# Kernel optimization log

Hardware: AMD Instinct MI355X
Metric: run time of the kernel (lower is better)

## Reference

```python
import jax, jax.numpy as jnp
import numpy as np

T, B, C = 2048, 8, 512
OUT = 512
NE = 16
TOPK = 2
LOSS_SCALE = 0.01
NEG_INF = 1.0e6  # module uses -1000000.0 for masked logits


def setup_inputs() -> dict:
    key = jax.random.key(0)
    k = jax.random.split(key, 4)
    a_assign = np.sqrt(6.0 / (C + NE)).astype(np.float32)  # xavier_uniform for Linear(C, NE)
    a_w1 = np.float32(np.sqrt(6.0) / (C + OUT))            # dynamic_init_method == 1
    return {
        "x": jax.random.normal(k[0], (T, B, C), dtype=jnp.float32),
        "assign_w": jax.random.uniform(k[1], (NE, C), minval=-a_assign, maxval=a_assign, dtype=jnp.float32),
        "assign_b": jnp.zeros((NE,), dtype=jnp.float32),
        "pw_w1": jax.random.uniform(k[2], (NE, OUT * C), minval=-a_w1, maxval=a_w1, dtype=jnp.float32),
        "bias_w": jnp.zeros((OUT, C), dtype=jnp.float32),  # pw_bias weight initialized to 0
        "bias_b": jnp.zeros((OUT,), dtype=jnp.float32),
    }


def reference(x, assign_w, assign_b, pw_w1, bias_w, bias_b):
    # key=None path of ConditionalDLFactorized18.forward, eval mode, tau=0 -> softmax gating.
    tokens = x.reshape(T * B, C)
    # Gating energies: Linear(key_dim, ne)
    energies = tokens @ assign_w.T + assign_b  # [TB, ne]
    # keeptopk_masked: set entries below k-th largest to -1e6
    topv, _ = jax.lax.top_k(energies, TOPK)
    energies = jnp.where(energies < topv[..., TOPK - 1:TOPK], -NEG_INF, energies)
    resp = jax.nn.softmax(energies, axis=-1)  # [TB, ne]
    # Importance/commitment loss (torch.std is unbiased -> ddof=1)
    importance = resp.sum(axis=0)  # [ne]
    loss = (LOSS_SCALE * jnp.std(importance, ddof=1) / jnp.mean(importance)).reshape(1)
    # Algebraically-equivalent reorder of (resp @ pw_w1).view(T,B,out,in) @ x:
    # apply each expert's matrix to the token first, then mix with resp.
    W = pw_w1.reshape(NE, OUT, C)
    expert_out = jnp.einsum("nc,eoc->neo", tokens, W)      # [TB, ne, out]
    y = jnp.einsum("ne,neo->no", resp, expert_out)          # [TB, out]
    y = y.reshape(T, B, OUT)
    # dynamic bias: pw_bias(x0) = x0 @ bias_w.T + bias_b
    y = y + x @ bias_w.T + bias_b
    return y, loss
```

## Files before the change

kernel.cpp:

```cpp
#include <hip/hip_runtime.h>
#include <hip/hip_bf16.h>

#define TB 16384
#define CDIM 512
#define OUTD 512
#define NE 16
#define NE_TOT 17
#define LOSS_SCALE 0.01f
#define BM 128
#define BN 128
#define BK 64
#define MAX_SCHED 144
#define MAXFLAG 8192
#define MARGIN 1e-3f

typedef __bf16 bf16_t;
typedef bf16_t bf16x8 __attribute__((ext_vector_type(8)));
typedef float f32x4 __attribute__((ext_vector_type(4)));
typedef unsigned short ushort4_t __attribute__((ext_vector_type(4)));
typedef unsigned short ushort8_t __attribute__((ext_vector_type(8)));

__device__ __forceinline__ unsigned short f2bf(float f) {
    unsigned int u = __float_as_uint(f);
    u += 0x7fffu + ((u >> 16) & 1u);
    return (unsigned short)(u >> 16);
}
__device__ __forceinline__ float bf2f(unsigned short h) {
    return __uint_as_float((unsigned int)h << 16);
}

__device__ __forceinline__ void async_copy16(void* lds, const void* g) {
    __builtin_amdgcn_global_load_lds(
        (const __attribute__((address_space(1))) unsigned int*)g,
        (__attribute__((address_space(3))) unsigned int*)lds, 16, 0, 0);
}

__global__ __launch_bounds__(256) void k_prep(
    const float* __restrict__ aw, unsigned short* __restrict__ awhl,
    int* cnt0, int* cnt1, float* importance, int* nflag, int* wflag)
{
    int t = threadIdx.x;
    if (t < NE) { cnt0[t] = 0; cnt1[t] = 0; importance[t] = 0.f; }
    if (t == 0) { *nflag = 0; *wflag = 0; }
    for (int i = t; i < NE * CDIM; i += 256) {
        float f = aw[i];
        unsigned short h = f2bf(f);
        float r = f - bf2f(h);
        awhl[i] = h;
        awhl[NE * CDIM + i] = f2bf(r);
    }
}

__global__ void k_wconv(const float* __restrict__ pw, const float* __restrict__ bw,
                        unsigned short* __restrict__ wbf, int* __restrict__ wflag) {
    long i = (long)blockIdx.x * 256 + threadIdx.x;
    const long NPW = (long)NE * OUTD * CDIM / 4;
    const long NTOT = (long)NE_TOT * OUTD * CDIM / 4;
    if (i >= NTOT) return;
    const float* src = (i < NPW) ? (pw + i * 4) : (bw + (i - NPW) * 4);
    float4 v = *(const float4*)src;
    ushort4_t o;
    o[0] = f2bf(v.x); o[1] = f2bf(v.y); o[2] = f2bf(v.z); o[3] = f2bf(v.w);
    *(ushort4_t*)(wbf + i * 4) = o;
    if (i >= NPW && (v.x != 0.f || v.y != 0.f || v.z != 0.f || v.w != 0.f))
        atomicOr(wflag, 1);
}

__global__ __launch_bounds__(256) void k_gate(
    const float* __restrict__ x, const unsigned short* __restrict__ awhl,
    const float* __restrict__ ab, unsigned short* __restrict__ xbf,
    int* __restrict__ dec, float2* __restrict__ respd,
    int* __restrict__ flaglist, int* __restrict__ nflag, float* __restrict__ importance)
{
    __shared__ float imp_s[NE];
    int tid = threadIdx.x;
    if (tid < NE) imp_s[tid] = 0.f;
    __syncthreads();

    int wv = tid >> 6, l = tid & 63;
    int n0 = blockIdx.x * 64 + wv * 16;
    int e = l & 15;
    int kg = l >> 4;

    const float* xrow = x + (size_t)(n0 + e) * CDIM + kg * 8;
    unsigned short* xbrow = xbf + (size_t)(n0 + e) * CDIM + kg * 8;
    const unsigned short* whiP = awhl + e * CDIM + kg * 8;
    const unsigned short* wloP = whiP + NE * CDIM;

    f32x4 acc = (f32x4){0.f, 0.f, 0.f, 0.f};
    #pragma unroll 4
    for (int ks = 0; ks < 16; ++ks) {
        float4 v0 = *(const float4*)(xrow + ks * 32);
        float4 v1 = *(const float4*)(xrow + ks * 32 + 4);
        ushort8_t hx, lx;
        #define CVT(idx, f) { unsigned short h_ = f2bf(f); hx[idx] = h_; \
                              float r_ = (f) - bf2f(h_); lx[idx] = f2bf(r_); }
        CVT(0, v0.x) CVT(1, v0.y) CVT(2, v0.z) CVT(3, v0.w)
        CVT(4, v1.x) CVT(5, v1.y) CVT(6, v1.z) CVT(7, v1.w)
        #undef CVT
        *(ushort8_t*)(xbrow + ks * 32) = hx;
        ushort8_t wh8 = *(const ushort8_t*)(whiP + ks * 32);
        ushort8_t wl8 = *(const ushort8_t*)(wloP + ks * 32);
        bf16x8 ah = *(bf16x8*)&hx, al = *(bf16x8*)&lx;
        bf16x8 bh = *(bf16x8*)&wh8, bl = *(bf16x8*)&wl8;
        acc = __builtin_amdgcn_mfma_f32_16x16x32_bf16(al, bh, acc, 0, 0, 0);
        acc = __builtin_amdgcn_mfma_f32_16x16x32_bf16(ah, bl, acc, 0, 0, 0);
        acc = __builtin_amdgcn_mfma_f32_16x16x32_bf16(ah, bh, acc, 0, 0, 0);
    }
    float bias = ab[e];
    f32x4 E;
    #pragma unroll
    for (int q = 0; q < 4; ++q) E[q] = acc[q] + bias;

    f32x4 m1 = E, m2, m3;
    #pragma unroll
    for (int q = 0; q < 4; ++q) { m2[q] = -3.4e38f; m3[q] = -3.4e38f; }
    #pragma unroll
    for (int off = 1; off <= 8; off <<= 1) {
        #pragma unroll
        for (int q = 0; q < 4; ++q) {
            float o1 = __shfl_xor(m1[q], off, 64);
            float o2 = __shfl_xor(m2[q], off, 64);
            float o3 = __shfl_xor(m3[q], off, 64);
            float M1 = fmaxf(m1[q], o1), x1 = fminf(m1[q], o1);
            float h2 = fmaxf(m2[q], o2), l2 = fminf(m2[q], o2);
            float M2 = fmaxf(x1, h2), x2 = fminf(x1, h2);
            float M3 = fmaxf(fmaxf(x2, l2), fmaxf(m3[q], o3));
            m1[q] = M1; m2[q] = M2; m3[q] = M3;
        }
    }
    f32x4 p, z;
    #pragma unroll
    for (int q = 0; q < 4; ++q) p[q] = (E[q] >= m2[q]) ? expf(E[q] - m1[q]) : 0.f;
    z = p;
    #pragma unroll
    for (int off = 1; off <= 8; off <<= 1)
        #pragma unroll
        for (int q = 0; q < 4; ++q) z[q] += __shfl_xor(z[q], off, 64);
    f32x4 resp;
    #pragma unroll
    for (int q = 0; q < 4; ++q) resp[q] = p[q] / z[q];

    int grp = l >> 4;
    int elo_q[4], ehi_q[4];
    float rlo_q[4], rhi_q[4];
    #pragma unroll
    for (int q = 0; q < 4; ++q) {
        unsigned long long mq = __ballot(p[q] > 0.f);
        unsigned int sub = (unsigned int)((mq >> (grp * 16)) & 0xffffULL);
        elo_q[q] = __builtin_ctz(sub);
        ehi_q[q] = 31 - __builtin_clz(sub);
        rlo_q[q] = __shfl(resp[q], grp * 16 + elo_q[q], 64);
        rhi_q[q] = __shfl(resp[q], grp * 16 + ehi_q[q], 64);
    }
    if ((l & 15) == 0) {
        #pragma unroll
        for (int q = 0; q < 4; ++q) {
            int n = n0 + grp * 4 + q;
            dec[n] = elo_q[q] | (ehi_q[q] << 8);
            respd[n] = make_float2(rlo_q[q], rhi_q[q]);
            if (m2[q] - m3[q] < MARGIN) {
                int ix = atomicAdd(nflag, 1);
                if (ix < MAXFLAG) flaglist[ix] = n;
            }
        }
    }
    float s = resp[0] + resp[1] + resp[2] + resp[3];
    s += __shfl_xor(s, 16, 64);
    s += __shfl_xor(s, 32, 64);
    if (l < 16) atomicAdd(&imp_s[e], s);
    __syncthreads();
    if (tid < NE) unsafeAtomicAdd(&importance[tid], imp_s[tid]);
}

__global__ __launch_bounds__(256) void k_repair(
    const float* __restrict__ x, const float* __restrict__ aw, const float* __restrict__ ab,
    const int* __restrict__ flaglist, const int* __restrict__ nflag,
    int* __restrict__ dec, float2* __restrict__ respd, float* __restrict__ importance)
{
    __shared__ double part[16][17];
    __shared__ double Ed[16];
    int tid = threadIdx.x;
    int e = tid >> 4, p = tid & 15;
    int nf = *nflag; if (nf > MAXFLAG) nf = MAXFLAG;
    for (int fi = blockIdx.x; fi < nf; fi += gridDim.x) {
        int n = flaglist[fi];
        const float* xp = x + (size_t)n * CDIM + p * 32;
        const float* wp = aw + e * CDIM + p * 32;
        double acc = 0.0;
        for (int j = 0; j < 32; ++j) acc = fma((double)xp[j], (double)wp[j], acc);
        part[e][p] = acc;
        __syncthreads();
        if (tid < 16) {
            double s = (double)ab[tid];
            for (int q = 0; q < 16; ++q) s += part[tid][q];
            Ed[tid] = s;
        }
        __syncthreads();
        if (tid == 0) {
            double m1 = -1e300, m2 = -1e300, m3 = -1e300;
            for (int q = 0; q < 16; ++q) {
                double v = Ed[q];
                if (v > m1) { m3 = m2; m2 = m1; m1 = v; }
                else if (v > m2) { m3 = m2; m2 = v; }
                else if (v > m3) { m3 = v; }
            }
            int elo = -1, ehi = -1;
            for (int q = 0; q < 16; ++q)
                if (Ed[q] >= m2) { if (elo < 0) elo = q; else ehi = q; }
            double plo = exp(Ed[elo] - m1), phi = exp(Ed[ehi] - m1);
            double zz = plo + phi;
            float rlo = (float)(plo / zz), rhi = (float)(phi / zz);
            int od = dec[n]; float2 orr = respd[n];
            unsafeAtomicAdd(&importance[od & 0xff], -orr.x);
            unsafeAtomicAdd(&importance[(od >> 8) & 0xff], -orr.y);
            unsafeAtomicAdd(&importance[elo], rlo);
            unsafeAtomicAdd(&importance[ehi], rhi);
            dec[n] = elo | (ehi << 8);
            respd[n] = make_float2(rlo, rhi);
        }
        __syncthreads();
    }
}

__global__ __launch_bounds__(256) void k_build(
    const int* __restrict__ dec, int* __restrict__ cnt0, int* __restrict__ cnt1,
    int* __restrict__ idx0, int* __restrict__ idx1)
{
    __shared__ int l0[NE], l1[NE], b0[NE], b1[NE];
    int tid = threadIdx.x;
    if (tid < NE) { l0[tid] = 0; l1[tid] = 0; }
    __syncthreads();
    int n = blockIdx.x * 256 + tid;
    int d = dec[n];
    int elo = d & 0xff, ehi = (d >> 8) & 0xff;
    int p0 = atomicAdd(&l0[elo], 1);
    int p1 = atomicAdd(&l1[ehi], 1);
    __syncthreads();
    if (tid < NE) {
        b0[tid] = atomicAdd(&cnt0[tid], l0[tid]);
        b1[tid] = atomicAdd(&cnt1[tid], l1[tid]);
    }
    __syncthreads();
    idx0[elo * TB + b0[elo] + p0] = n;
    idx1[ehi * TB + b1[ehi] + p1] = n;
}

__global__ void k_finish(const float* __restrict__ importance, float* __restrict__ out_loss,
                         const int* __restrict__ cnt0, const int* __restrict__ cnt1,
                         int* __restrict__ sched0, int* __restrict__ sched1,
                         int* __restrict__ sn0, int* __restrict__ sn1) {
    int l = threadIdx.x;
    if (l < 64) {
        float v = (l < NE) ? importance[l] : 0.f;
        float s = v;
        #pragma unroll
        for (int off = 8; off >= 1; off >>= 1) s += __shfl_xor(s, off, 64);
        float mean = s / 16.f;
        float d = (l < NE) ? (v - mean) : 0.f;
        float ss = d * d;
        #pragma unroll
        for (int off = 8; off >= 1; off >>= 1) ss += __shfl_xor(ss, off, 64);
        if (l == 0) {
            float stdv = sqrtf(ss / 15.f);
            out_loss[0] = LOSS_SCALE * stdv / mean;
        }
    } else if (l == 64) {
        int p = 0;
        for (int e = 0; e < NE; ++e) {
            int nb = (cnt0[e] + BM - 1) / BM;
            for (int i = 0; i < nb; ++i) sched0[p++] = (e << 16) | i;
        }
        *sn0 = p;
    } else if (l == 65) {
        int p = 0;
        for (int e = 0; e < NE; ++e) {
            int nb = (cnt1[e] + BM - 1) / BM;
            for (int i = 0; i < nb; ++i) sched1[p++] = (e << 16) | i;
        }
        *sn1 = p;
    }
}

template<int RANK>
__global__ __launch_bounds__(256) void k_gemm(
    const unsigned short* __restrict__ xbf, const unsigned short* __restrict__ wbf,
    const int* __restrict__ cnts, const int* __restrict__ idx,
    const float2* __restrict__ respd, const int* __restrict__ sched,
    const int* __restrict__ sn, const float* __restrict__ bias_b, float* __restrict__ y)
{
    if ((int)blockIdx.y >= *sn) return;
    int s = sched[blockIdx.y];
    int e = s >> 16, m0 = (s & 0xffff) * BM, cnt = cnts[e];
    int n0 = blockIdx.x * BN;
    int tid = threadIdx.x;
    int wave = tid >> 6, lane = tid & 63;
    int wm = wave >> 1, wn = wave & 1;
    int fr = lane & 15, fq = lane >> 4;

    __shared__ unsigned short As[BM * BK];
    __shared__ unsigned short Bs[BN * BK];

    const int* my_idx = idx + e * TB;

    f32x4 acc[4][4];
    #pragma unroll
    for (int m = 0; m < 4; ++m)
        #pragma unroll
        for (int nn = 0; nn < 4; ++nn) acc[m][nn] = (f32x4){0.f, 0.f, 0.f, 0.f};

    int srow = wave * 8 + (lane >> 3);
    int cg = lane & 7;
    const unsigned short* aSrc[4];
    const unsigned short* bSrc[4];
    #pragma unroll
    for (int c = 0; c < 4; ++c) {
        int row = c * 32 + srow;
        int sc = (cg ^ (row & 7)) * 8;
        int rr = m0 + row; if (rr >= cnt) rr = cnt - 1;
        int tok = my_idx[rr];
        aSrc[c] = xbf + (size_t)tok * CDIM + sc;
        bSrc[c] = wbf + ((size_t)e * OUTD + n0 + row) * CDIM + sc;
    }
    for (int k0 = 0; k0 < CDIM; k0 += BK) {
        __syncthreads();
        #pragma unroll
        for (int c = 0; c < 4; ++c) {
            async_copy16(&As[(c * 32 + wave * 8) * BK], aSrc[c] + k0);
            async_copy16(&Bs[(c * 32 + wave * 8) * BK], bSrc[c] + k0);
        }
        __syncthreads();
        #pragma unroll
        for (int ss = 0; ss < 2; ++ss) {
            bf16x8 af[4], bv[4];
            #pragma unroll
            for (int m = 0; m < 4; ++m) {
                int row = wm * 64 + m * 16 + fr;
                int ch = ((ss * 4 + fq) ^ (row & 7)) * 8;
                af[m] = *(const bf16x8*)(&As[row * BK + ch]);
            }
            #pragma unroll
            for (int nn = 0; nn < 4; ++nn) {
                int row = wn * 64 + nn * 16 + fr;
                int ch = ((ss * 4 + fq) ^ (row & 7)) * 8;
                bv[nn] = *(const bf16x8*)(&Bs[row * BK + ch]);
            }
            #pragma unroll
            for (int m = 0; m < 4; ++m)
                #pragma unroll
                for (int nn = 0; nn < 4; ++nn)
                    acc[m][nn] = __builtin_amdgcn_mfma_f32_16x16x32_bf16(af[m], bv[nn], acc[m][nn], 0, 0, 0);
        }
    }

    float bb[4];
    if (RANK == 0) {
        #pragma unroll
        for (int nn = 0; nn < 4; ++nn) bb[nn] = bias_b[n0 + wn * 64 + nn * 16 + fr];
    }
    #pragma unroll
    for (int m = 0; m < 4; ++m)
        #pragma unroll
        for (int q = 0; q < 4; ++q) {
            int r = m0 + wm * 64 + m * 16 + fq * 4 + q;
            if (r < cnt) {
                int tok = my_idx[r];
                float2 rp = respd[tok];
                float w = (RANK == 0) ? rp.x : rp.y;
                float* yrow = y + (size_t)tok * OUTD + n0 + wn * 64 + fr;
                #pragma unroll
                for (int nn = 0; nn < 4; ++nn) {
                    if (RANK == 0) yrow[nn * 16] = fmaf(w, acc[m][nn][q], bb[nn]);
                    else           yrow[nn * 16] += w * acc[m][nn][q];
                }
            }
        }
}

__global__ __launch_bounds__(256) void k_dense(
    const unsigned short* __restrict__ xbf, const unsigned short* __restrict__ wbf,
    const int* __restrict__ wflag, float* __restrict__ y)
{
    if (*wflag == 0) return;
    int e = NE;
    int m0 = blockIdx.y * BM;
    int n0 = blockIdx.x * BN;
    int tid = threadIdx.x;
    int wave = tid >> 6, lane = tid & 63;
    int wm = wave >> 1, wn = wave & 1;
    int fr = lane & 15, fq = lane >> 4;

    __shared__ unsigned short As[BM * BK];
    __shared__ unsigned short Bs[BN * BK];

    f32x4 acc[4][4];
    #pragma unroll
    for (int m = 0; m < 4; ++m)
        #pragma unroll
        for (int nn = 0; nn < 4; ++nn) acc[m][nn] = (f32x4){0.f, 0.f, 0.f, 0.f};

    int srow = wave * 8 + (lane >> 3);
    int cg = lane & 7;
    const unsigned short* aSrc[4];
    const unsigned short* bSrc[4];
    #pragma unroll
    for (int c = 0; c < 4; ++c) {
        int row = c * 32 + srow;
        int sc = (cg ^ (row & 7)) * 8;
        aSrc[c] = xbf + (size_t)(m0 + row) * CDIM + sc;
        bSrc[c] = wbf + ((size_t)e * OUTD + n0 + row) * CDIM + sc;
    }
    for (int k0 = 0; k0 < CDIM; k0 += BK) {
        __syncthreads();
        #pragma unroll
        for (int c = 0; c < 4; ++c) {
            async_copy16(&As[(c * 32 + wave * 8) * BK], aSrc[c] + k0);
            async_copy16(&Bs[(c * 32 + wave * 8) * BK], bSrc[c] + k0);
        }
        __syncthreads();
        #pragma unroll
        for (int ss = 0; ss < 2; ++ss) {
            bf16x8 af[4], bv[4];
            #pragma unroll
            for (int m = 0; m < 4; ++m) {
                int row = wm * 64 + m * 16 + fr;
                int ch = ((ss * 4 + fq) ^ (row & 7)) * 8;
                af[m] = *(const bf16x8*)(&As[row * BK + ch]);
            }
            #pragma unroll
            for (int nn = 0; nn < 4; ++nn) {
                int row = wn * 64 + nn * 16 + fr;
                int ch = ((ss * 4 + fq) ^ (row & 7)) * 8;
                bv[nn] = *(const bf16x8*)(&Bs[row * BK + ch]);
            }
            #pragma unroll
            for (int m = 0; m < 4; ++m)
                #pragma unroll
                for (int nn = 0; nn < 4; ++nn)
                    acc[m][nn] = __builtin_amdgcn_mfma_f32_16x16x32_bf16(af[m], bv[nn], acc[m][nn], 0, 0, 0);
        }
    }
    #pragma unroll
    for (int m = 0; m < 4; ++m)
        #pragma unroll
        for (int q = 0; q < 4; ++q) {
            int r = m0 + wm * 64 + m * 16 + fq * 4 + q;
            float* yrow = y + (size_t)r * OUTD + n0 + wn * 64 + fr;
            #pragma unroll
            for (int nn = 0; nn < 4; ++nn) yrow[nn * 16] += acc[m][nn][q];
        }
}

extern "C" void kernel_launch(void* const* d_in, const int* in_sizes, int n_in,
                              void* d_out, int out_size, void* d_ws, size_t ws_size,
                              hipStream_t stream) {
    const float* x        = (const float*)d_in[0];
    const float* assign_w = (const float*)d_in[1];
    const float* assign_b = (const float*)d_in[2];
    const float* pw_w1    = (const float*)d_in[3];
    const float* bias_w   = (const float*)d_in[4];
    const float* bias_b   = (const float*)d_in[5];
    float* y    = (float*)d_out;
    float* loss = y + (size_t)TB * OUTD;

    char* ws = (char*)d_ws;
    unsigned short* xbf  = (unsigned short*)(ws);
    unsigned short* wbf  = (unsigned short*)(ws + 16777216);
    int*    idx0      = (int*)   (ws + 25690112);
    int*    idx1      = (int*)   (ws + 26738688);
    int*    dec       = (int*)   (ws + 27787264);
    float2* respd     = (float2*)(ws + 27852800);
    int*    flaglist  = (int*)   (ws + 27983872);
    unsigned short* awhl = (unsigned short*)(ws + 28016640);
    char*   misc      = ws + 28049408;
    int*    cnt0      = (int*)   (misc + 0);
    int*    cnt1      = (int*)   (misc + 64);
    float*  importance= (float*) (misc + 128);
    int*    nflag     = (int*)   (misc + 192);
    int*    wflag     = (int*)   (misc + 196);
    int*    sn0       = (int*)   (misc + 200);
    int*    sn1       = (int*)   (misc + 204);
    int*    sched0    = (int*)   (misc + 256);
    int*    sched1    = (int*)   (misc + 896);

    k_prep<<<1, 256, 0, stream>>>(assign_w, awhl, cnt0, cnt1, importance, nflag, wflag);
    k_wconv<<<(NE_TOT * OUTD * CDIM / 4 + 255) / 256, 256, 0, stream>>>(pw_w1, bias_w, wbf, wflag);
    k_gate<<<TB / 64, 256, 0, stream>>>(x, awhl, assign_b, xbf, dec, respd,
                                        flaglist, nflag, importance);
    k_repair<<<32, 256, 0, stream>>>(x, assign_w, assign_b, flaglist, nflag,
                                     dec, respd, importance);
    k_build<<<TB / 256, 256, 0, stream>>>(dec, cnt0, cnt1, idx0, idx1);
    k_finish<<<1, 128, 0, stream>>>(importance, loss, cnt0, cnt1, sched0, sched1, sn0, sn1);
    k_gemm<0><<<dim3(OUTD / BN, MAX_SCHED), 256, 0, stream>>>(
        xbf, wbf, cnt0, idx0, respd, sched0, sn0, bias_b, y);
    k_gemm<1><<<dim3(OUTD / BN, MAX_SCHED), 256, 0, stream>>>(
        xbf, wbf, cnt1, idx1, respd, sched1, sn1, bias_b, y);
    k_dense<<<dim3(OUTD / BN, TB / BM), 256, 0, stream>>>(xbf, wbf, wflag, y);
}
```

Before: 130.6 us.

## Group tokens by expert pair and fuse both expert GEMMs into one kernel

Tokens are bucketed by their (top1, top2) expert pair using count, scan and scatter kernels instead of per-rank expert lists. A single GEMM kernel then computes both experts' outputs for each tile, reusing the gathered activation rows, and writes y once. This removes the second GEMM launch and its read-modify-write pass over y. It also adds double-buffered LDS staging to overlap loads with MFMA work. With up to 240 possible pairs the tiles are less full, so more padded rows are wasted, and the kernel holds two accumulator sets, which raises register pressure.

New measurement: 172.2 us. 1.32x slower.

```diff
diff --git a/kernel.cpp b/kernel.cpp
--- a/kernel.cpp
+++ b/kernel.cpp
@@ -10,7 +10,7 @@
 #define BM 128
 #define BN 128
 #define BK 64
-#define MAX_SCHED 144
+#define MAX_SCHED_P 320
 #define MAXFLAG 8192
 #define MARGIN 1e-3f
 
@@ -37,10 +37,11 @@
 
 __global__ __launch_bounds__(256) void k_prep(
     const float* __restrict__ aw, unsigned short* __restrict__ awhl,
-    int* cnt0, int* cnt1, float* importance, int* nflag, int* wflag)
+    int* pair_cnt, float* importance, int* nflag, int* wflag)
 {
     int t = threadIdx.x;
-    if (t < NE) { cnt0[t] = 0; cnt1[t] = 0; importance[t] = 0.f; }
+    pair_cnt[t] = 0;
+    if (t < NE) importance[t] = 0.f;
     if (t == 0) { *nflag = 0; *wflag = 0; }
     for (int i = t; i < NE * CDIM; i += 256) {
         float f = aw[i];
@@ -223,35 +224,42 @@
     }
 }
 
-__global__ __launch_bounds__(256) void k_build(
-    const int* __restrict__ dec, int* __restrict__ cnt0, int* __restrict__ cnt1,
-    int* __restrict__ idx0, int* __restrict__ idx1)
-{
-    __shared__ int l0[NE], l1[NE], b0[NE], b1[NE];
+__global__ __launch_bounds__(256) void k_count(
+    const int* __restrict__ dec, int* __restrict__ pair_cnt)
+{
+    __shared__ int c_s[256];
     int tid = threadIdx.x;
-    if (tid < NE) { l0[tid] = 0; l1[tid] = 0; }
+    c_s[tid] = 0;
     __syncthreads();
     int n = blockIdx.x * 256 + tid;
     int d = dec[n];
-    int elo = d & 0xff, ehi = (d >> 8) & 0xff;
-    int p0 = atomicAdd(&l0[elo], 1);
-    int p1 = atomicAdd(&l1[ehi], 1);
+    int pid = ((d & 0xff) << 4) | ((d >> 8) & 0xff);
+    atomicAdd(&c_s[pid], 1);
     __syncthreads();
-    if (tid < NE) {
-        b0[tid] = atomicAdd(&cnt0[tid], l0[tid]);
-        b1[tid] = atomicAdd(&cnt1[tid], l1[tid]);
-    }
-    __syncthreads();
-    idx0[elo * TB + b0[elo] + p0] = n;
-    idx1[ehi * TB + b1[ehi] + p1] = n;
-}
-
-__global__ void k_finish(const float* __restrict__ importance, float* __restrict__ out_loss,
-                         const int* __restrict__ cnt0, const int* __restrict__ cnt1,
-                         int* __restrict__ sched0, int* __restrict__ sched1,
-                         int* __restrict__ sn0, int* __restrict__ sn1) {
-    int l = threadIdx.x;
-    if (l < 64) {
+    if (c_s[tid] > 0) atomicAdd(&pair_cnt[tid], c_s[tid]);
+}
+
+__global__ void k_scan(const int* __restrict__ pair_cnt, int* __restrict__ pair_base,
+                       int* __restrict__ pair_fill, int* __restrict__ sched,
+                       int* __restrict__ sn,
+                       const float* __restrict__ importance, float* __restrict__ out_loss)
+{
+    __shared__ int base_s[256];
+    int t = threadIdx.x;
+    if (t == 0) {
+        int p = 0;
+        for (int i = 0; i < 256; ++i) { base_s[i] = p; p += pair_cnt[i]; }
+    }
+    if (t == 1) {
+        int ns = 0;
+        for (int i = 0; i < 256; ++i) {
+            int nb = (pair_cnt[i] + BM - 1) / BM;
+            for (int b = 0; b < nb; ++b) sched[ns++] = (i << 8) | b;
+        }
+        *sn = ns;
+    }
+    if (t >= 64 && t < 128) {
+        int l = t - 64;
         float v = (l < NE) ? importance[l] : 0.f;
         float s = v;
         #pragma unroll
@@ -265,54 +273,58 @@
             float stdv = sqrtf(ss / 15.f);
             out_loss[0] = LOSS_SCALE * stdv / mean;
         }
-    } else if (l == 64) {
-        int p = 0;
-        for (int e = 0; e < NE; ++e) {
-            int nb = (cnt0[e] + BM - 1) / BM;
-            for (int i = 0; i < nb; ++i) sched0[p++] = (e << 16) | i;
-        }
-        *sn0 = p;
-    } else if (l == 65) {
-        int p = 0;
-        for (int e = 0; e < NE; ++e) {
-            int nb = (cnt1[e] + BM - 1) / BM;
-            for (int i = 0; i < nb; ++i) sched1[p++] = (e << 16) | i;
-        }
-        *sn1 = p;
-    }
-}
-
-template<int RANK>
-__global__ __launch_bounds__(256) void k_gemm(
+    }
+    __syncthreads();
+    pair_base[t] = base_s[t];
+    pair_fill[t] = base_s[t];
+}
+
+__global__ __launch_bounds__(256) void k_scatter(
+    const int* __restrict__ dec, int* __restrict__ pair_fill, int* __restrict__ pidx)
+{
+    int n = blockIdx.x * 256 + threadIdx.x;
+    int d = dec[n];
+    int pid = ((d & 0xff) << 4) | ((d >> 8) & 0xff);
+    int slot = atomicAdd(&pair_fill[pid], 1);
+    pidx[slot] = n;
+}
+
+__global__ __launch_bounds__(256) void k_gemm_pair(
     const unsigned short* __restrict__ xbf, const unsigned short* __restrict__ wbf,
-    const int* __restrict__ cnts, const int* __restrict__ idx,
-    const float2* __restrict__ respd, const int* __restrict__ sched,
-    const int* __restrict__ sn, const float* __restrict__ bias_b, float* __restrict__ y)
+    const int* __restrict__ pair_cnt, const int* __restrict__ pair_base,
+    const int* __restrict__ pidx, const float2* __restrict__ respd,
+    const int* __restrict__ sched, const int* __restrict__ sn,
+    const float* __restrict__ bias_b, float* __restrict__ y)
 {
     if ((int)blockIdx.y >= *sn) return;
     int s = sched[blockIdx.y];
-    int e = s >> 16, m0 = (s & 0xffff) * BM, cnt = cnts[e];
+    int pid = s >> 8, mb = s & 0xff;
+    int e0 = pid >> 4, e1 = pid & 15;
+    int cnt = pair_cnt[pid];
+    int m0 = mb * BM;
+    const int* my_idx = pidx + pair_base[pid];
     int n0 = blockIdx.x * BN;
     int tid = threadIdx.x;
     int wave = tid >> 6, lane = tid & 63;
     int wm = wave >> 1, wn = wave & 1;
     int fr = lane & 15, fq = lane >> 4;
 
-    __shared__ unsigned short As[BM * BK];
-    __shared__ unsigned short Bs[BN * BK];
-
-    const int* my_idx = idx + e * TB;
-
-    f32x4 acc[4][4];
+    __shared__ unsigned short As[2][BM * BK];
+    __shared__ unsigned short Bs[2][BM * BK];
+
+    f32x4 acc0[4][4], acc1[4][4];
     #pragma unroll
     for (int m = 0; m < 4; ++m)
         #pragma unroll
-        for (int nn = 0; nn < 4; ++nn) acc[m][nn] = (f32x4){0.f, 0.f, 0.f, 0.f};
+        for (int nn = 0; nn < 4; ++nn) {
+            acc0[m][nn] = (f32x4){0.f, 0.f, 0.f, 0.f};
+            acc1[m][nn] = (f32x4){0.f, 0.f, 0.f, 0.f};
+        }
 
     int srow = wave * 8 + (lane >> 3);
     int cg = lane & 7;
     const unsigned short* aSrc[4];
-    const unsigned short* bSrc[4];
+    size_t bOff[4];
     #pragma unroll
     for (int c = 0; c < 4; ++c) {
         int row = c * 32 + srow;
@@ -320,16 +332,19 @@
         int rr = m0 + row; if (rr >= cnt) rr = cnt - 1;
         int tok = my_idx[rr];
         aSrc[c] = xbf + (size_t)tok * CDIM + sc;
-        bSrc[c] = wbf + ((size_t)e * OUTD + n0 + row) * CDIM + sc;
-    }
-    for (int k0 = 0; k0 < CDIM; k0 += BK) {
-        __syncthreads();
+        bOff[c] = (size_t)(n0 + row) * CDIM + sc;
+    }
+    const unsigned short* wb0 = wbf + (size_t)e0 * OUTD * CDIM;
+    const unsigned short* wb1 = wbf + (size_t)e1 * OUTD * CDIM;
+
+    auto stagef = [&](int buf, const unsigned short* wb, int k0) {
         #pragma unroll
         for (int c = 0; c < 4; ++c) {
-            async_copy16(&As[(c * 32 + wave * 8) * BK], aSrc[c] + k0);
-            async_copy16(&Bs[(c * 32 + wave * 8) * BK], bSrc[c] + k0);
-        }
-        __syncthreads();
+            async_copy16(&As[buf][(c * 32 + wave * 8) * BK], aSrc[c] + k0);
+            async_copy16(&Bs[buf][(c * 32 + wave * 8) * BK], wb + bOff[c] + k0);
+        }
+    };
+    auto compute = [&](int cb, f32x4 (&acc)[4][4]) {
         #pragma unroll
         for (int ss = 0; ss < 2; ++ss) {
             bf16x8 af[4], bv[4];
@@ -337,13 +352,13 @@
             for (int m = 0; m < 4; ++m) {
                 int row = wm * 64 + m * 16 + fr;
                 int ch = ((ss * 4 + fq) ^ (row & 7)) * 8;
-                af[m] = *(const bf16x8*)(&As[row * BK + ch]);
+                af[m] = *(const bf16x8*)(&As[cb][row * BK + ch]);
             }
             #pragma unroll
             for (int nn = 0; nn < 4; ++nn) {
                 int row = wn * 64 + nn * 16 + fr;
                 int ch = ((ss * 4 + fq) ^ (row & 7)) * 8;
-                bv[nn] = *(const bf16x8*)(&Bs[row * BK + ch]);
+                bv[nn] = *(const bf16x8*)(&Bs[cb][row * BK + ch]);
             }
             #pragma unroll
             for (int m = 0; m < 4; ++m)
@@ -351,13 +366,28 @@
                 for (int nn = 0; nn < 4; ++nn)
                     acc[m][nn] = __builtin_amdgcn_mfma_f32_16x16x32_bf16(af[m], bv[nn], acc[m][nn], 0, 0, 0);
         }
+    };
+
+    stagef(0, wb0, 0);
+    __syncthreads();
+    int cur = 0;
+    for (int t = 0; t < 8; ++t) {
+        if (t < 7) stagef(cur ^ 1, wb0, (t + 1) * BK);
+        else       stagef(cur ^ 1, wb1, 0);
+        compute(cur, acc0);
+        __syncthreads();
+        cur ^= 1;
+    }
+    for (int t = 0; t < 8; ++t) {
+        if (t < 7) stagef(cur ^ 1, wb1, (t + 1) * BK);
+        compute(cur, acc1);
+        __syncthreads();
+        cur ^= 1;
     }
 
     float bb[4];
-    if (RANK == 0) {
-        #pragma unroll
-        for (int nn = 0; nn < 4; ++nn) bb[nn] = bias_b[n0 + wn * 64 + nn * 16 + fr];
-    }
+    #pragma unroll
+    for (int nn = 0; nn < 4; ++nn) bb[nn] = bias_b[n0 + wn * 64 + nn * 16 + fr];
     #pragma unroll
     for (int m = 0; m < 4; ++m)
         #pragma unroll
@@ -366,13 +396,11 @@
             if (r < cnt) {
                 int tok = my_idx[r];
                 float2 rp = respd[tok];
-                float w = (RANK == 0) ? rp.x : rp.y;
                 float* yrow = y + (size_t)tok * OUTD + n0 + wn * 64 + fr;
                 #pragma unroll
-                for (int nn = 0; nn < 4; ++nn) {
-                    if (RANK == 0) yrow[nn * 16] = fmaf(w, acc[m][nn][q], bb[nn]);
-                    else           yrow[nn * 16] += w * acc[m][nn][q];
-                }
+                for (int nn = 0; nn < 4; ++nn)
+                    yrow[nn * 16] = fmaf(rp.x, acc0[m][nn][q],
+                                    fmaf(rp.y, acc1[m][nn][q], bb[nn]));
             }
         }
 }
@@ -391,7 +419,7 @@
     int fr = lane & 15, fq = lane >> 4;
 
     __shared__ unsigned short As[BM * BK];
-    __shared__ unsigned short Bs[BN * BK];
+    __shared__ unsigned short Bs[BM * BK];
 
     f32x4 acc[4][4];
     #pragma unroll
@@ -466,34 +494,32 @@
     char* ws = (char*)d_ws;
     unsigned short* xbf  = (unsigned short*)(ws);
     unsigned short* wbf  = (unsigned short*)(ws + 16777216);
-    int*    idx0      = (int*)   (ws + 25690112);
-    int*    idx1      = (int*)   (ws + 26738688);
+    int*    pidx      = (int*)   (ws + 25690112);
     int*    dec       = (int*)   (ws + 27787264);
     float2* respd     = (float2*)(ws + 27852800);
     int*    flaglist  = (int*)   (ws + 27983872);
     unsigned short* awhl = (unsigned short*)(ws + 28016640);
     char*   misc      = ws + 28049408;
-    int*    cnt0      = (int*)   (misc + 0);
-    int*    cnt1      = (int*)   (misc + 64);
-    float*  importance= (float*) (misc + 128);
-    int*    nflag     = (int*)   (misc + 192);
-    int*    wflag     = (int*)   (misc + 196);
-    int*    sn0       = (int*)   (misc + 200);
-    int*    sn1       = (int*)   (misc + 204);
-    int*    sched0    = (int*)   (misc + 256);
-    int*    sched1    = (int*)   (misc + 896);
-
-    k_prep<<<1, 256, 0, stream>>>(assign_w, awhl, cnt0, cnt1, importance, nflag, wflag);
+    int*    pair_cnt  = (int*)   (misc + 0);
+    int*    pair_base = (int*)   (misc + 1024);
+    int*    pair_fill = (int*)   (misc + 2048);
+    float*  importance= (float*) (misc + 3072);
+    int*    nflag     = (int*)   (misc + 3136);
+    int*    wflag     = (int*)   (misc + 3140);
+    int*    sn        = (int*)   (misc + 3144);
+    int*    sched     = (int*)   (misc + 3200);
+
+    k_prep<<<1, 256, 0, stream>>>(assign_w, awhl, pair_cnt, importance, nflag, wflag);
     k_wconv<<<(NE_TOT * OUTD * CDIM / 4 + 255) / 256, 256, 0, stream>>>(pw_w1, bias_w, wbf, wflag);
     k_gate<<<TB / 64, 256, 0, stream>>>(x, awhl, assign_b, xbf, dec, respd,
                                         flaglist, nflag, importance);
     k_repair<<<32, 256, 0, stream>>>(x, assign_w, assign_b, flaglist, nflag,
                                      dec, respd, importance);
-    k_build<<<TB / 256, 256, 0, stream>>>(dec, cnt0, cnt1, idx0, idx1);
-    k_finish<<<1, 128, 0, stream>>>(importance, loss, cnt0, cnt1, sched0, sched1, sn0, sn1);
-    k_gemm<0><<<dim3(OUTD / BN, MAX_SCHED), 256, 0, stream>>>(
-        xbf, wbf, cnt0, idx0, respd, sched0, sn0, bias_b, y);
-    k_gemm<1><<<dim3(OUTD / BN, MAX_SCHED), 256, 0, stream>>>(
-        xbf, wbf, cnt1, idx1, respd, sched1, sn1, bias_b, y);
+    k_count<<<TB / 256, 256, 0, stream>>>(dec, pair_cnt);
+    k_scan<<<1, 256, 0, stream>>>(pair_cnt, pair_base, pair_fill, sched, sn,
+                                  importance, loss);
+    k_scatter<<<TB / 256, 256, 0, stream>>>(dec, pair_fill, pidx);
+    k_gemm_pair<<<dim3(OUTD / BN, MAX_SCHED_P), 256, 0, stream>>>(
+        xbf, wbf, pair_cnt, pair_base, pidx, respd, sched, sn, bias_b, y);
     k_dense<<<dim3(OUTD / BN, TB / BM), 256, 0, stream>>>(xbf, wbf, wflag, y);
 }
```

## Double-buffer LDS tiles and halve N tile in expert GEMM kernels

Applied to the files above, without the earlier changes.

Both the routed expert GEMM and the dense GEMM now use two LDS buffers, so the async copy of the next K slice is issued before the current slice is computed. This removes one barrier per iteration and overlaps global loads with MFMA work. BN is cut from 128 to 64, which doubles the block count and halves the accumulator registers per wave. The cost is that each block reads the gathered A rows twice as often relative to its output, and per-block arithmetic intensity drops.

Result: slower. 142.4 us (+9.0%).

```diff
diff --git a/kernel.cpp b/kernel.cpp
--- a/kernel.cpp
+++ b/kernel.cpp
@@ -8,7 +8,7 @@
 #define NE_TOT 17
 #define LOSS_SCALE 0.01f
 #define BM 128
-#define BN 128
+#define BN 64
 #define BK 64
 #define MAX_SCHED 144
 #define MAXFLAG 8192
@@ -298,21 +298,21 @@
     int wm = wave >> 1, wn = wave & 1;
     int fr = lane & 15, fq = lane >> 4;
 
-    __shared__ unsigned short As[BM * BK];
-    __shared__ unsigned short Bs[BN * BK];
+    __shared__ unsigned short As[2][BM * BK];
+    __shared__ unsigned short Bs[2][BN * BK];
 
     const int* my_idx = idx + e * TB;
 
-    f32x4 acc[4][4];
+    f32x4 acc[4][2];
     #pragma unroll
     for (int m = 0; m < 4; ++m)
         #pragma unroll
-        for (int nn = 0; nn < 4; ++nn) acc[m][nn] = (f32x4){0.f, 0.f, 0.f, 0.f};
+        for (int nn = 0; nn < 2; ++nn) acc[m][nn] = (f32x4){0.f, 0.f, 0.f, 0.f};
 
     int srow = wave * 8 + (lane >> 3);
     int cg = lane & 7;
     const unsigned short* aSrc[4];
-    const unsigned short* bSrc[4];
+    const unsigned short* bSrc[2];
     #pragma unroll
     for (int c = 0; c < 4; ++c) {
         int row = c * 32 + srow;
@@ -320,43 +320,61 @@
         int rr = m0 + row; if (rr >= cnt) rr = cnt - 1;
         int tok = my_idx[rr];
         aSrc[c] = xbf + (size_t)tok * CDIM + sc;
+    }
+    #pragma unroll
+    for (int c = 0; c < 2; ++c) {
+        int row = c * 32 + srow;
+        int sc = (cg ^ (row & 7)) * 8;
         bSrc[c] = wbf + ((size_t)e * OUTD + n0 + row) * CDIM + sc;
     }
-    for (int k0 = 0; k0 < CDIM; k0 += BK) {
-        __syncthreads();
-        #pragma unroll
-        for (int c = 0; c < 4; ++c) {
-            async_copy16(&As[(c * 32 + wave * 8) * BK], aSrc[c] + k0);
-            async_copy16(&Bs[(c * 32 + wave * 8) * BK], bSrc[c] + k0);
-        }
-        __syncthreads();
+
+    auto stagef = [&](int buf, int k0) {
+        #pragma unroll
+        for (int c = 0; c < 4; ++c)
+            async_copy16(&As[buf][(c * 32 + wave * 8) * BK], aSrc[c] + k0);
+        #pragma unroll
+        for (int c = 0; c < 2; ++c)
+            async_copy16(&Bs[buf][(c * 32 + wave * 8) * BK], bSrc[c] + k0);
+    };
+    auto compute = [&](int cb) {
         #pragma unroll
         for (int ss = 0; ss < 2; ++ss) {
-            bf16x8 af[4], bv[4];
+            bf16x8 af[4], bv[2];
             #pragma unroll
             for (int m = 0; m < 4; ++m) {
                 int row = wm * 64 + m * 16 + fr;
                 int ch = ((ss * 4 + fq) ^ (row & 7)) * 8;
-                af[m] = *(const bf16x8*)(&As[row * BK + ch]);
-            }
-            #pragma unroll
-            for (int nn = 0; nn < 4; ++nn) {
-                int row = wn * 64 + nn * 16 + fr;
+                af[m] = *(const bf16x8*)(&As[cb][row * BK + ch]);
+            }
+            #pragma unroll
+            for (int nn = 0; nn < 2; ++nn) {
+                int row = wn * 32 + nn * 16 + fr;
                 int ch = ((ss * 4 + fq) ^ (row & 7)) * 8;
-                bv[nn] = *(const bf16x8*)(&Bs[row * BK + ch]);
+                bv[nn] = *(const bf16x8*)(&Bs[cb][row * BK + ch]);
             }
             #pragma unroll
             for (int m = 0; m < 4; ++m)
                 #pragma unroll
-                for (int nn = 0; nn < 4; ++nn)
+                for (int nn = 0; nn < 2; ++nn)
                     acc[m][nn] = __builtin_amdgcn_mfma_f32_16x16x32_bf16(af[m], bv[nn], acc[m][nn], 0, 0, 0);
         }
-    }
-
-    float bb[4];
+    };
+
+    stagef(0, 0);
+    __syncthreads();
+    int cur = 0;
+    #pragma unroll
+    for (int t = 0; t < 8; ++t) {
+        if (t < 7) stagef(cur ^ 1, (t + 1) * BK);
+        compute(cur);
+        __syncthreads();
+        cur ^= 1;
+    }
+
+    float bb[2];
     if (RANK == 0) {
         #pragma unroll
-        for (int nn = 0; nn < 4; ++nn) bb[nn] = bias_b[n0 + wn * 64 + nn * 16 + fr];
+        for (int nn = 0; nn < 2; ++nn) bb[nn] = bias_b[n0 + wn * 32 + nn * 16 + fr];
     }
     #pragma unroll
     for (int m = 0; m < 4; ++m)
@@ -367,9 +385,9 @@
                 int tok = my_idx[r];
                 float2 rp = respd[tok];
                 float w = (RANK == 0) ? rp.x : rp.y;
-                float* yrow = y + (size_t)tok * OUTD + n0 + wn * 64 + fr;
+                float* yrow = y + (size_t)tok * OUTD + n0 + wn * 32 + fr;
                 #pragma unroll
-                for (int nn = 0; nn < 4; ++nn) {
+                for (int nn = 0; nn < 2; ++nn) {
                     if (RANK == 0) yrow[nn * 16] = fmaf(w, acc[m][nn][q], bb[nn]);
                     else           yrow[nn * 16] += w * acc[m][nn][q];
                 }
@@ -390,64 +408,80 @@
     int wm = wave >> 1, wn = wave & 1;
     int fr = lane & 15, fq = lane >> 4;
 
-    __shared__ unsigned short As[BM * BK];
-    __shared__ unsigned short Bs[BN * BK];
-
-    f32x4 acc[4][4];
+    __shared__ unsigned short As[2][BM * BK];
+    __shared__ unsigned short Bs[2][BN * BK];
+
+    f32x4 acc[4][2];
     #pragma unroll
     for (int m = 0; m < 4; ++m)
         #pragma unroll
-        for (int nn = 0; nn < 4; ++nn) acc[m][nn] = (f32x4){0.f, 0.f, 0.f, 0.f};
+        for (int nn = 0; nn < 2; ++nn) acc[m][nn] = (f32x4){0.f, 0.f, 0.f, 0.f};
 
     int srow = wave * 8 + (lane >> 3);
     int cg = lane & 7;
     const unsigned short* aSrc[4];
-    const unsigned short* bSrc[4];
+    const unsigned short* bSrc[2];
     #pragma unroll
     for (int c = 0; c < 4; ++c) {
         int row = c * 32 + srow;
         int sc = (cg ^ (row & 7)) * 8;
         aSrc[c] = xbf + (size_t)(m0 + row) * CDIM + sc;
+    }
+    #pragma unroll
+    for (int c = 0; c < 2; ++c) {
+        int row = c * 32 + srow;
+        int sc = (cg ^ (row & 7)) * 8;
         bSrc[c] = wbf + ((size_t)e * OUTD + n0 + row) * CDIM + sc;
     }
-    for (int k0 = 0; k0 < CDIM; k0 += BK) {
-        __syncthreads();
-        #pragma unroll
-        for (int c = 0; c < 4; ++c) {
-            async_copy16(&As[(c * 32 + wave * 8) * BK], aSrc[c] + k0);
-            async_copy16(&Bs[(c * 32 + wave * 8) * BK], bSrc[c] + k0);
-        }
-        __syncthreads();
+    auto stagef = [&](int buf, int k0) {
+        #pragma unroll
+        for (int c = 0; c < 4; ++c)
+            async_copy16(&As[buf][(c * 32 + wave * 8) * BK], aSrc[c] + k0);
+        #pragma unroll
+        for (int c = 0; c < 2; ++c)
+            async_copy16(&Bs[buf][(c * 32 + wave * 8) * BK], bSrc[c] + k0);
+    };
+    auto compute = [&](int cb) {
         #pragma unroll
         for (int ss = 0; ss < 2; ++ss) {
-            bf16x8 af[4], bv[4];
+            bf16x8 af[4], bv[2];
             #pragma unroll
             for (int m = 0; m < 4; ++m) {
                 int row = wm * 64 + m * 16 + fr;
                 int ch = ((ss * 4 + fq) ^ (row & 7)) * 8;
-                af[m] = *(const bf16x8*)(&As[row * BK + ch]);
-            }
-            #pragma unroll
-            for (int nn = 0; nn < 4; ++nn) {
-                int row = wn * 64 + nn * 16 + fr;
+                af[m] = *(const bf16x8*)(&As[cb][row * BK + ch]);
+            }
+            #pragma unroll
+            for (int nn = 0; nn < 2; ++nn) {
+                int row = wn * 32 + nn * 16 + fr;
                 int ch = ((ss * 4 + fq) ^ (row & 7)) * 8;
-                bv[nn] = *(const bf16x8*)(&Bs[row * BK + ch]);
+                bv[nn] = *(const bf16x8*)(&Bs[cb][row * BK + ch]);
             }
             #pragma unroll
             for (int m = 0; m < 4; ++m)
                 #pragma unroll
-                for (int nn = 0; nn < 4; ++nn)
+                for (int nn = 0; nn < 2; ++nn)
                     acc[m][nn] = __builtin_amdgcn_mfma_f32_16x16x32_bf16(af[m], bv[nn], acc[m][nn], 0, 0, 0);
         }
+    };
+    stagef(0, 0);
+    __syncthreads();
+    int cur = 0;
+    #pragma unroll
+    for (int t = 0; t < 8; ++t) {
+        if (t < 7) stagef(cur ^ 1, (t + 1) * BK);
+        compute(cur);
+        __syncthreads();
+        cur ^= 1;
     }
     #pragma unroll
     for (int m = 0; m < 4; ++m)
         #pragma unroll
         for (int q = 0; q < 4; ++q) {
             int r = m0 + wm * 64 + m * 16 + fq * 4 + q;
-            float* yrow = y + (size_t)r * OUTD + n0 + wn * 64 + fr;
-            #pragma unroll
-            for (int nn = 0; nn < 4; ++nn) yrow[nn * 16] += acc[m][nn][q];
+            float* yrow = y + (size_t)r * OUTD + n0 + wn * 32 + fr;
+            #pragma unroll
+            for (int nn = 0; nn < 2; ++nn) yrow[nn * 16] += acc[m][nn][q];
         }
 }
 
```

## Pipeline expert GEMM with 4-stage async LDS buffers and smaller tiles

Applied to the files above, without the earlier changes.

Rewrites the grouped expert GEMM to use a 4-buffer async-copy pipeline with explicit vmcnt waits and a single barrier per K step, in place of the load-sync-compute loop. The tile shrinks from 128x128x64 to 128x64x32, which doubles the block count along N. The grid is transposed so that schedule entries sharing a weight tile run adjacently. The dense bias-path kernel becomes a mode of the same template. The aim is to overlap global loads with MFMA work and raise occupancy, at the cost of more loads of the gathered A rows per output and smaller per-block reuse.

New measurement: 135.8 us. +4.0%, slower.

```diff
diff --git a/kernel.cpp b/kernel.cpp
--- a/kernel.cpp
+++ b/kernel.cpp
@@ -8,8 +8,9 @@
 #define NE_TOT 17
 #define LOSS_SCALE 0.01f
 #define BM 128
-#define BN 128
-#define BK 64
+#define BN 64
+#define BK 32
+#define NSTEP 16
 #define MAX_SCHED 144
 #define MAXFLAG 8192
 #define MARGIN 1e-3f
@@ -282,81 +283,100 @@
     }
 }
 
-template<int RANK>
+template<int MODE>
 __global__ __launch_bounds__(256) void k_gemm(
     const unsigned short* __restrict__ xbf, const unsigned short* __restrict__ wbf,
     const int* __restrict__ cnts, const int* __restrict__ idx,
     const float2* __restrict__ respd, const int* __restrict__ sched,
-    const int* __restrict__ sn, const float* __restrict__ bias_b, float* __restrict__ y)
+    const int* __restrict__ sn, const int* __restrict__ wflag,
+    const float* __restrict__ bias_b, float* __restrict__ y)
 {
-    if ((int)blockIdx.y >= *sn) return;
-    int s = sched[blockIdx.y];
-    int e = s >> 16, m0 = (s & 0xffff) * BM, cnt = cnts[e];
-    int n0 = blockIdx.x * BN;
+    int e, m0, cnt;
+    const int* my_idx = nullptr;
+    if (MODE == 2) {
+        if (*wflag == 0) return;
+        e = NE; m0 = blockIdx.x * BM; cnt = TB;
+    } else {
+        if ((int)blockIdx.x >= *sn) return;
+        int s = sched[blockIdx.x];
+        e = s >> 16; m0 = (s & 0xffff) * BM; cnt = cnts[e];
+        my_idx = idx + e * TB;
+    }
+    int n0 = blockIdx.y * BN;
     int tid = threadIdx.x;
     int wave = tid >> 6, lane = tid & 63;
     int wm = wave >> 1, wn = wave & 1;
     int fr = lane & 15, fq = lane >> 4;
 
-    __shared__ unsigned short As[BM * BK];
-    __shared__ unsigned short Bs[BN * BK];
-
-    const int* my_idx = idx + e * TB;
-
-    f32x4 acc[4][4];
+    __shared__ unsigned short As[4][BM * BK];
+    __shared__ unsigned short Bs[4][BN * BK];
+
+    f32x4 acc[4][2];
     #pragma unroll
     for (int m = 0; m < 4; ++m)
         #pragma unroll
-        for (int nn = 0; nn < 4; ++nn) acc[m][nn] = (f32x4){0.f, 0.f, 0.f, 0.f};
-
-    int srow = wave * 8 + (lane >> 3);
-    int cg = lane & 7;
-    const unsigned short* aSrc[4];
-    const unsigned short* bSrc[4];
-    #pragma unroll
-    for (int c = 0; c < 4; ++c) {
-        int row = c * 32 + srow;
-        int sc = (cg ^ (row & 7)) * 8;
-        int rr = m0 + row; if (rr >= cnt) rr = cnt - 1;
-        int tok = my_idx[rr];
-        aSrc[c] = xbf + (size_t)tok * CDIM + sc;
-        bSrc[c] = wbf + ((size_t)e * OUTD + n0 + row) * CDIM + sc;
-    }
-    for (int k0 = 0; k0 < CDIM; k0 += BK) {
-        __syncthreads();
-        #pragma unroll
-        for (int c = 0; c < 4; ++c) {
-            async_copy16(&As[(c * 32 + wave * 8) * BK], aSrc[c] + k0);
-            async_copy16(&Bs[(c * 32 + wave * 8) * BK], bSrc[c] + k0);
-        }
-        __syncthreads();
-        #pragma unroll
-        for (int ss = 0; ss < 2; ++ss) {
-            bf16x8 af[4], bv[4];
+        for (int nn = 0; nn < 2; ++nn) acc[m][nn] = (f32x4){0.f, 0.f, 0.f, 0.f};
+
+    int rl = lane >> 2, cc = lane & 3;
+    int swz = (cc ^ (rl & 3)) * 8;
+    int rowA0 = wave * 32 + rl;
+    int rowA1 = rowA0 + 16;
+    int tok0, tok1;
+    if (MODE == 2) { tok0 = m0 + rowA0; tok1 = m0 + rowA1; }
+    else {
+        int rr0 = m0 + rowA0; if (rr0 >= cnt) rr0 = cnt - 1;
+        int rr1 = m0 + rowA1; if (rr1 >= cnt) rr1 = cnt - 1;
+        tok0 = my_idx[rr0]; tok1 = my_idx[rr1];
+    }
+    const unsigned short* aS0 = xbf + (size_t)tok0 * CDIM + swz;
+    const unsigned short* aS1 = xbf + (size_t)tok1 * CDIM + swz;
+    const unsigned short* bS0 = wbf + ((size_t)e * OUTD + n0 + wave * 16 + rl) * CDIM + swz;
+
+    unsigned short* dA0 = &As[0][(wave * 32) * BK];
+    unsigned short* dA1 = &As[0][(wave * 32 + 16) * BK];
+    unsigned short* dB0 = &Bs[0][(wave * 16) * BK];
+    const int ASTRIDE = BM * BK, BSTRIDE = BN * BK;
+
+    auto stage = [&](int buf, int t) {
+        async_copy16(dA0 + buf * ASTRIDE, aS0 + t * BK);
+        async_copy16(dA1 + buf * ASTRIDE, aS1 + t * BK);
+        async_copy16(dB0 + buf * BSTRIDE, bS0 + t * BK);
+    };
+    auto compute = [&](int cb) {
+        bf16x8 af[4], bv[2];
+        #pragma unroll
+        for (int m = 0; m < 4; ++m) {
+            int row = wm * 64 + m * 16 + fr;
+            af[m] = *(const bf16x8*)(&As[cb][row * BK + ((fq ^ (row & 3)) * 8)]);
+        }
+        #pragma unroll
+        for (int nn = 0; nn < 2; ++nn) {
+            int row = wn * 32 + nn * 16 + fr;
+            bv[nn] = *(const bf16x8*)(&Bs[cb][row * BK + ((fq ^ (row & 3)) * 8)]);
+        }
+        #pragma unroll
+        for (int m = 0; m < 4; ++m)
             #pragma unroll
-            for (int m = 0; m < 4; ++m) {
-                int row = wm * 64 + m * 16 + fr;
-                int ch = ((ss * 4 + fq) ^ (row & 7)) * 8;
-                af[m] = *(const bf16x8*)(&As[row * BK + ch]);
-            }
-            #pragma unroll
-            for (int nn = 0; nn < 4; ++nn) {
-                int row = wn * 64 + nn * 16 + fr;
-                int ch = ((ss * 4 + fq) ^ (row & 7)) * 8;
-                bv[nn] = *(const bf16x8*)(&Bs[row * BK + ch]);
-            }
-            #pragma unroll
-            for (int m = 0; m < 4; ++m)
-                #pragma unroll
-                for (int nn = 0; nn < 4; ++nn)
-                    acc[m][nn] = __builtin_amdgcn_mfma_f32_16x16x32_bf16(af[m], bv[nn], acc[m][nn], 0, 0, 0);
-        }
-    }
-
-    float bb[4];
-    if (RANK == 0) {
-        #pragma unroll
-        for (int nn = 0; nn < 4; ++nn) bb[nn] = bias_b[n0 + wn * 64 + nn * 16 + fr];
+            for (int nn = 0; nn < 2; ++nn)
+                acc[m][nn] = __builtin_amdgcn_mfma_f32_16x16x32_bf16(af[m], bv[nn], acc[m][nn], 0, 0, 0);
+    };
+
+    stage(0, 0); stage(1, 1); stage(2, 2);
+    #pragma unroll
+    for (int t = 0; t < NSTEP; ++t) {
+        if (t <= NSTEP - 3)      asm volatile("s_waitcnt vmcnt(6)" ::: "memory");
+        else if (t == NSTEP - 2) asm volatile("s_waitcnt vmcnt(3)" ::: "memory");
+        else                     asm volatile("s_waitcnt vmcnt(0)" ::: "memory");
+        __builtin_amdgcn_sched_barrier(0);
+        __builtin_amdgcn_s_barrier();
+        compute(t & 3);
+        if (t <= NSTEP - 4) stage((t + 3) & 3, t + 3);
+    }
+
+    float bb[2];
+    if (MODE == 0) {
+        #pragma unroll
+        for (int nn = 0; nn < 2; ++nn) bb[nn] = bias_b[n0 + wn * 32 + nn * 16 + fr];
     }
     #pragma unroll
     for (int m = 0; m < 4; ++m)
@@ -364,90 +384,23 @@
         for (int q = 0; q < 4; ++q) {
             int r = m0 + wm * 64 + m * 16 + fq * 4 + q;
             if (r < cnt) {
-                int tok = my_idx[r];
-                float2 rp = respd[tok];
-                float w = (RANK == 0) ? rp.x : rp.y;
-                float* yrow = y + (size_t)tok * OUTD + n0 + wn * 64 + fr;
+                float* yrow;
+                float w = 1.f;
+                if (MODE == 2) {
+                    yrow = y + (size_t)r * OUTD + n0 + wn * 32 + fr;
+                } else {
+                    int tok = my_idx[r];
+                    float2 rp = respd[tok];
+                    w = (MODE == 0) ? rp.x : rp.y;
+                    yrow = y + (size_t)tok * OUTD + n0 + wn * 32 + fr;
+                }
                 #pragma unroll
-                for (int nn = 0; nn < 4; ++nn) {
-                    if (RANK == 0) yrow[nn * 16] = fmaf(w, acc[m][nn][q], bb[nn]);
-                    else           yrow[nn * 16] += w * acc[m][nn][q];
+                for (int nn = 0; nn < 2; ++nn) {
+                    if (MODE == 0) yrow[nn * 16] = fmaf(w, acc[m][nn][q], bb[nn]);
+                    else if (MODE == 1) yrow[nn * 16] += w * acc[m][nn][q];
+                    else yrow[nn * 16] += acc[m][nn][q];
                 }
             }
-        }
-}
-
-__global__ __launch_bounds__(256) void k_dense(
-    const unsigned short* __restrict__ xbf, const unsigned short* __restrict__ wbf,
-    const int* __restrict__ wflag, float* __restrict__ y)
-{
-    if (*wflag == 0) return;
-    int e = NE;
-    int m0 = blockIdx.y * BM;
-    int n0 = blockIdx.x * BN;
-    int tid = threadIdx.x;
-    int wave = tid >> 6, lane = tid & 63;
-    int wm = wave >> 1, wn = wave & 1;
-    int fr = lane & 15, fq = lane >> 4;
-
-    __shared__ unsigned short As[BM * BK];
-    __shared__ unsigned short Bs[BN * BK];
-
-    f32x4 acc[4][4];
-    #pragma unroll
-    for (int m = 0; m < 4; ++m)
-        #pragma unroll
-        for (int nn = 0; nn < 4; ++nn) acc[m][nn] = (f32x4){0.f, 0.f, 0.f, 0.f};
-
-    int srow = wave * 8 + (lane >> 3);
-    int cg = lane & 7;
-    const unsigned short* aSrc[4];
-    const unsigned short* bSrc[4];
-    #pragma unroll
-    for (int c = 0; c < 4; ++c) {
-        int row = c * 32 + srow;
-        int sc = (cg ^ (row & 7)) * 8;
-        aSrc[c] = xbf + (size_t)(m0 + row) * CDIM + sc;
-        bSrc[c] = wbf + ((size_t)e * OUTD + n0 + row) * CDIM + sc;
-    }
-    for (int k0 = 0; k0 < CDIM; k0 += BK) {
-        __syncthreads();
-        #pragma unroll
-        for (int c = 0; c < 4; ++c) {
-            async_copy16(&As[(c * 32 + wave * 8) * BK], aSrc[c] + k0);
-            async_copy16(&Bs[(c * 32 + wave * 8) * BK], bSrc[c] + k0);
-        }
-        __syncthreads();
-        #pragma unroll
-        for (int ss = 0; ss < 2; ++ss) {
-            bf16x8 af[4], bv[4];
-            #pragma unroll
-            for (int m = 0; m < 4; ++m) {
-                int row = wm * 64 + m * 16 + fr;
-                int ch = ((ss * 4 + fq) ^ (row & 7)) * 8;
-                af[m] = *(const bf16x8*)(&As[row * BK + ch]);
-            }
-            #pragma unroll
-            for (int nn = 0; nn < 4; ++nn) {
-                int row = wn * 64 + nn * 16 + fr;
-                int ch = ((ss * 4 + fq) ^ (row & 7)) * 8;
-                bv[nn] = *(const bf16x8*)(&Bs[row * BK + ch]);
-            }
-            #pragma unroll
-            for (int m = 0; m < 4; ++m)
-                #pragma unroll
-                for (int nn = 0; nn < 4; ++nn)
-                    acc[m][nn] = __builtin_amdgcn_mfma_f32_16x16x32_bf16(af[m], bv[nn], acc[m][nn], 0, 0, 0);
-        }
-    }
-    #pragma unroll
-    for (int m = 0; m < 4; ++m)
-        #pragma unroll
-        for (int q = 0; q < 4; ++q) {
-            int r = m0 + wm * 64 + m * 16 + fq * 4 + q;
-            float* yrow = y + (size_t)r * OUTD + n0 + wn * 64 + fr;
-            #pragma unroll
-            for (int nn = 0; nn < 4; ++nn) yrow[nn * 16] += acc[m][nn][q];
         }
 }
 
@@ -491,9 +444,10 @@
                                      dec, respd, importance);
     k_build<<<TB / 256, 256, 0, stream>>>(dec, cnt0, cnt1, idx0, idx1);
     k_finish<<<1, 128, 0, stream>>>(importance, loss, cnt0, cnt1, sched0, sched1, sn0, sn1);
-    k_gemm<0><<<dim3(OUTD / BN, MAX_SCHED), 256, 0, stream>>>(
-        xbf, wbf, cnt0, idx0, respd, sched0, sn0, bias_b, y);
-    k_gemm<1><<<dim3(OUTD / BN, MAX_SCHED), 256, 0, stream>>>(
-        xbf, wbf, cnt1, idx1, respd, sched1, sn1, bias_b, y);
-    k_dense<<<dim3(OUTD / BN, TB / BM), 256, 0, stream>>>(xbf, wbf, wflag, y);
-}
+    k_gemm<0><<<dim3(MAX_SCHED, OUTD / BN), 256, 0, stream>>>(
+        xbf, wbf, cnt0, idx0, respd, sched0, sn0, wflag, bias_b, y);
+    k_gemm<1><<<dim3(MAX_SCHED, OUTD / BN), 256, 0, stream>>>(
+        xbf, wbf, cnt1, idx1, respd, sched1, sn1, wflag, bias_b, y);
+    k_gemm<2><<<dim3(TB / BM, OUTD / BN), 256, 0, stream>>>(
+        xbf, wbf, cnt0, idx0, respd, sched0, sn0, wflag, bias_b, y);
+}
```
